# Performance work log

Hardware: AMD Instinct MI355X
Metric: run time of the kernel (lower is better)

Reference implementation:

```python
import jax, jax.numpy as jnp
import numpy as np
import math

DIM = 2048
N_HEADS = 16
N_KV_HEADS = 8
HEAD_DIM = DIM // N_HEADS  # 128
N_REP = N_HEADS // N_KV_HEADS  # 2
BLOCK = 128
TOPK = 8
NEG_INF = -10000.0
SEQ = 4096
BS = 1


def _rope_tables(seq_len, head_dim, base=10000.0):
    inv_freq = 1.0 / (base ** (jnp.arange(0, head_dim, 2, dtype=jnp.float32) / head_dim))
    ang = jnp.arange(seq_len, dtype=jnp.float32)[:, None] * inv_freq[None, :]  # [S, hd/2]
    return jnp.cos(ang), jnp.sin(ang)


def _apply_rope(t, cos, sin):
    # t: [bs, S, h, hd]; interleaved pairs
    t1 = t[..., 0::2]
    t2 = t[..., 1::2]
    c = cos[None, :, None, :]
    s = sin[None, :, None, :]
    out_even = t1 * c - t2 * s
    out_odd = t1 * s + t2 * c
    out = jnp.stack([out_even, out_odd], axis=-1)  # [bs,S,h,hd/2,2]
    return out.reshape(t.shape)


def setup_inputs() -> dict:
    key = jax.random.key(0)
    ks = jax.random.split(key, 5)
    scale = 1.0 / math.sqrt(DIM)
    x = jax.random.normal(ks[0], (BS, SEQ, DIM), dtype=jnp.float32)
    wq = jax.random.normal(ks[1], (DIM, N_HEADS * HEAD_DIM), dtype=jnp.float32) * scale
    wk = jax.random.normal(ks[2], (DIM, N_KV_HEADS * HEAD_DIM), dtype=jnp.float32) * scale
    wv = jax.random.normal(ks[3], (DIM, N_KV_HEADS * HEAD_DIM), dtype=jnp.float32) * scale
    wo = jax.random.normal(ks[4], (DIM, DIM), dtype=jnp.float32) * scale
    return {"x": x, "wq": wq, "wk": wk, "wv": wv, "wo": wo}


def reference(x, wq, wk, wv, wo):
    bs, S, _ = x.shape
    inv_sqrt_d = 1.0 / math.sqrt(HEAD_DIM)

    q = (x @ wq).reshape(bs, S, N_HEADS, HEAD_DIM)
    k = (x @ wk).reshape(bs, S, N_KV_HEADS, HEAD_DIM)
    v = (x @ wv).reshape(bs, S, N_KV_HEADS, HEAD_DIM)

    cos, sin = _rope_tables(S, HEAD_DIM)
    q = _apply_rope(q, cos, sin)
    k = _apply_rope(k, cos, sin)

    # [bs, h, S, hd]
    q = jnp.transpose(q, (0, 2, 1, 3))
    k = jnp.transpose(k, (0, 2, 1, 3))
    v = jnp.transpose(v, (0, 2, 1, 3))

    # GQA expand (repeat_interleave over head dim)
    k_e = jnp.repeat(k, N_REP, axis=1)
    v_e = jnp.repeat(v, N_REP, axis=1)

    num_blocks = S // BLOCK  # 32, divides evenly (pad_len == 0)
    k_blocks = k_e.reshape(bs, N_HEADS, num_blocks, BLOCK, HEAD_DIM)
    block_means = k_blocks.mean(axis=3)  # [bs,h,nb,hd]

    gating = jnp.einsum('bhsd,bhnd->bhsn', q, block_means) * inv_sqrt_d
    q_block_idx = jnp.arange(S) // BLOCK
    future_block = q_block_idx[:, None] < jnp.arange(num_blocks)[None, :]  # [S, nb]
    gating = jnp.where(future_block[None, None], NEG_INF, gating)

    curr_k = min(TOPK, num_blocks)
    _, sel_idx = jax.lax.top_k(gating, curr_k)  # [bs,h,S,k]
    selected = jnp.sum(jax.nn.one_hot(sel_idx, num_blocks, dtype=jnp.float32), axis=-2) > 0  # [bs,h,S,nb]

    token_keep = jnp.repeat(selected, BLOCK, axis=-1)[..., :S]  # [bs,h,S,S]
    token_mask = jnp.where(token_keep, 0.0, NEG_INF)

    scores = jnp.einsum('bhsd,bhtd->bhst', q, k_e) * inv_sqrt_d
    causal = jnp.triu(jnp.ones((S, S), dtype=jnp.float32), k=1)  # 1 where future token
    # faithful to source: elementwise max of token mask and causal*neg_inf
    final_mask = jnp.maximum(token_mask, causal[None, None] * NEG_INF)
    scores = scores + final_mask

    probs = jax.nn.softmax(scores.astype(jnp.float32), axis=-1).astype(scores.dtype)
    out = jnp.einsum('bhst,bhtd->bhsd', probs, v_e)
    out = jnp.transpose(out, (0, 2, 1, 3)).reshape(bs, S, N_HEADS * HEAD_DIM)
    return out @ wo
```

## Files before the change

kernel.cpp:

```cpp
#include <hip/hip_runtime.h>
#include <hip/hip_fp16.h>

#define SQ   4096
#define DIMM 2048
#define QKVN 4096

typedef unsigned short u16;
typedef unsigned int u32;
typedef __attribute__((ext_vector_type(8))) short    short8;
typedef __attribute__((ext_vector_type(8))) _Float16 half8;
typedef __attribute__((ext_vector_type(4))) float    f32x4;

__device__ __forceinline__ u16 f2bf(float f) {
  u32 u = __float_as_uint(f);
  u32 r = u + 0x7fffu + ((u >> 16) & 1u);
  return (u16)(r >> 16);
}
__device__ __forceinline__ float bf2f(u16 h) { return __uint_as_float(((u32)h) << 16); }
__device__ __forceinline__ u16 f2h(float f) { return __half_as_ushort(__float2half(f)); }
__device__ __forceinline__ float h2f(u16 h) { union { u16 u; _Float16 f; } c; c.u = h; return (float)c.f; }

__device__ __forceinline__ void gll16(const void* g, void* l) {
  __builtin_amdgcn_global_load_lds((const __attribute__((address_space(1))) void*)g,
                                   (__attribute__((address_space(3))) void*)l, 16, 0, 0);
}

__device__ __host__ __forceinline__ int cidx(int qb) {
  return qb < 8 ? qb : qb < 16 ? 8 + (qb - 8) * 2 : qb < 24 ? 24 + (qb - 16) * 3 : 48 + (qb - 24) * 4;
}

__global__ __launch_bounds__(256) void k_tables(float* __restrict__ cosb, float* __restrict__ sinb) {
  int idx = blockIdx.x * 256 + threadIdx.x;
  int pos = idx >> 6, i = idx & 63;
  double f = 1.0 / pow(10000.0, (double)i / 64.0);
  float inv = (float)f;
  float ang = (float)pos * inv;
  cosb[idx] = (float)cos((double)ang);
  sinb[idx] = (float)sin((double)ang);
}

__global__ __launch_bounds__(256) void k_split_x(const float* __restrict__ x,
                                                 u16* __restrict__ xh, u16* __restrict__ xl) {
  size_t base = ((size_t)blockIdx.x * 256 + threadIdx.x) * 4;
  float4 v = *(const float4*)(x + base);
  float vv[4] = {v.x, v.y, v.z, v.w};
  u16 hh[4], ll[4];
#pragma unroll
  for (int j = 0; j < 4; j++) {
    hh[j] = f2bf(vv[j]);
    ll[j] = f2bf(vv[j] - bf2f(hh[j]));
  }
  *(uint2*)(xh + base) = make_uint2((u32)hh[0] | ((u32)hh[1] << 16), (u32)hh[2] | ((u32)hh[3] << 16));
  *(uint2*)(xl + base) = make_uint2((u32)ll[0] | ((u32)ll[1] << 16), (u32)ll[2] | ((u32)ll[3] << 16));
}

__global__ __launch_bounds__(256) void k_trans_split(const float* __restrict__ src, int N,
                                                     u16* __restrict__ dh, u16* __restrict__ dl,
                                                     int rowOff) {
  __shared__ float t[64][65];
  int n0 = blockIdx.x * 64, k0 = blockIdx.y * 64;
  int tid = threadIdx.x;
  int c = tid & 63, r4 = tid >> 6;
#pragma unroll
  for (int it = 0; it < 16; it++) {
    int kk = it * 4 + r4;
    t[kk][c] = src[(size_t)(k0 + kk) * N + n0 + c];
  }
  __syncthreads();
#pragma unroll
  for (int it = 0; it < 16; it++) {
    int nn = it * 4 + r4;
    float v = t[c][nn];
    u16 hh = f2bf(v);
    size_t o = (size_t)(rowOff + n0 + nn) * 2048 + k0 + c;
    dh[o] = hh;
    dl[o] = f2bf(v - bf2f(hh));
  }
}

__global__ __launch_bounds__(256) void k_trans_f16(const float* __restrict__ src, int N,
                                                   u16* __restrict__ dst) {
  __shared__ float t[64][65];
  int n0 = blockIdx.x * 64, k0 = blockIdx.y * 64;
  int tid = threadIdx.x;
  int c = tid & 63, r4 = tid >> 6;
#pragma unroll
  for (int it = 0; it < 16; it++) {
    int kk = it * 4 + r4;
    t[kk][c] = src[(size_t)(k0 + kk) * N + n0 + c];
  }
  __syncthreads();
#pragma unroll
  for (int it = 0; it < 16; it++) {
    int nn = it * 4 + r4;
    dst[(size_t)(n0 + nn) * 2048 + k0 + c] = f2h(t[c][nn]);
  }
}

__global__ __launch_bounds__(256) void k_gemm_qkv(
    const u16* __restrict__ xh, const u16* __restrict__ xl,
    const u16* __restrict__ wth, const u16* __restrict__ wtl,
    float* __restrict__ qkv) {
  __shared__ u16 lds[4 * 128 * 64];
  const int tid = threadIdx.x;
  const int lane = tid & 63, wid = tid >> 6;
  const int rg = lane >> 4, c16 = lane & 15;
  const int bid0 = blockIdx.y * 32 + blockIdx.x;
  const int swz = (bid0 & 7) * 128 + (bid0 >> 3);
  const int m0 = (swz >> 5) * 128, n0 = (swz & 31) * 128;
  const int wm = wid >> 1, wn = wid & 1;
  const u16* gsrc = (wid == 0) ? xh + (size_t)m0 * 2048
                  : (wid == 1) ? xl + (size_t)m0 * 2048
                  : (wid == 2) ? wth + (size_t)n0 * 2048
                               : wtl + (size_t)n0 * 2048;
  u16* ldsm = lds + wid * 8192;
  const int sr = lane >> 3, scn = lane & 7;

  f32x4 acc[4][4];
#pragma unroll
  for (int a = 0; a < 4; a++)
#pragma unroll
    for (int b = 0; b < 4; b++) acc[a][b] = (f32x4){0.f, 0.f, 0.f, 0.f};

  for (int k0 = 0; k0 < 2048; k0 += 64) {
#pragma unroll
    for (int i = 0; i < 16; i++) {
      int r = i * 8 + sr;
      int cs = (scn ^ (r & 7)) * 8;
      gll16(gsrc + (size_t)r * 2048 + k0 + cs, ldsm + i * 512);
    }
    __syncthreads();
#pragma unroll
    for (int kk = 0; kk < 2; kk++) {
      short8 ah[4], al[4], bh[4], bl[4];
      int ch = kk * 4 + rg;
#pragma unroll
      for (int mf = 0; mf < 4; mf++) {
        int m = wm * 64 + mf * 16 + c16;
        int off = m * 64 + ((ch ^ (m & 7)) * 8);
        ah[mf] = *(const short8*)(lds + off);
        al[mf] = *(const short8*)(lds + 8192 + off);
      }
#pragma unroll
      for (int nf = 0; nf < 4; nf++) {
        int n = wn * 64 + nf * 16 + c16;
        int off = n * 64 + ((ch ^ (n & 7)) * 8);
        bh[nf] = *(const short8*)(lds + 16384 + off);
        bl[nf] = *(const short8*)(lds + 24576 + off);
      }
#pragma unroll
      for (int mf = 0; mf < 4; mf++)
#pragma unroll
        for (int nf = 0; nf < 4; nf++) {
          acc[mf][nf] = __builtin_amdgcn_mfma_f32_16x16x32_bf16(ah[mf], bh[nf], acc[mf][nf], 0, 0, 0);
          acc[mf][nf] = __builtin_amdgcn_mfma_f32_16x16x32_bf16(ah[mf], bl[nf], acc[mf][nf], 0, 0, 0);
          acc[mf][nf] = __builtin_amdgcn_mfma_f32_16x16x32_bf16(al[mf], bh[nf], acc[mf][nf], 0, 0, 0);
        }
    }
    __syncthreads();
  }
#pragma unroll
  for (int mf = 0; mf < 4; mf++)
#pragma unroll
    for (int nf = 0; nf < 4; nf++)
#pragma unroll
      for (int j = 0; j < 4; j++) {
        int m = m0 + wm * 64 + mf * 16 + rg * 4 + j;
        int n = n0 + wn * 64 + nf * 16 + c16;
        qkv[(size_t)m * QKVN + n] = acc[mf][nf][j];
      }
}

__global__ __launch_bounds__(256) void k_rope_qk(const float* __restrict__ qkv,
                                                 const float* __restrict__ cosb,
                                                 const float* __restrict__ sinb,
                                                 u16* __restrict__ qf, u16* __restrict__ kf2) {
  int idx = blockIdx.x * 256 + threadIdx.x;
  int i = idx & 63;
  int th = idx >> 6;
  int h = th % 24, t = th / 24;
  int c0 = (h < 16) ? h * 128 + 2 * i : 2048 + (h - 16) * 128 + 2 * i;
  float2 eo = *(const float2*)(qkv + (size_t)t * QKVN + c0);
  float c = cosb[t * 64 + i], s = sinb[t * 64 + i];
  float re = eo.x * c - eo.y * s;
  float ro = eo.x * s + eo.y * c;
  if (h < 16) {
    const float QSC = (float)(1.4426950408889634 * 0.08838834764831843);
    u32 pk = (u32)f2h(re * QSC) | ((u32)f2h(ro * QSC) << 16);
    *(u32*)(qf + ((size_t)h * SQ + t) * 128 + 2 * i) = pk;
  } else {
    int hk = h - 16;
    int d = 2 * i;
    int tile = t >> 6, tok = t & 63;
    int kk = tok >> 5, t5 = tok & 31;
    int hf = (t5 >> 2) & 1, c16v = ((t5 >> 3) << 2) | (t5 & 3);
    int dk = d >> 5, rg = (d >> 3) & 3, e = d & 7;
    int lane = rg * 16 + c16v, f = (kk * 2 + hf) * 4 + dk;
    u32 pk = (u32)f2h(re) | ((u32)f2h(ro) << 16);
    *(u32*)(kf2 + ((size_t)((hk * 64 + tile) * 16 + f) * 64 + lane) * 8 + e) = pk;
  }
}

__global__ __launch_bounds__(64) void k_bm(const float* __restrict__ qkv,
                                           const float* __restrict__ cosb,
                                           const float* __restrict__ sinb,
                                           float* __restrict__ bm) {
  int hk = blockIdx.x >> 5, n = blockIdx.x & 31;
  int i = threadIdx.x;
  double se = 0.0, so = 0.0;
  for (int t = 0; t < 128; t++) {
    int tt = n * 128 + t;
    float2 eo = *(const float2*)(qkv + (size_t)tt * QKVN + 2048 + hk * 128 + 2 * i);
    float c = cosb[tt * 64 + i], s = sinb[tt * 64 + i];
    se += (double)(eo.x * c - eo.y * s);
    so += (double)(eo.x * s + eo.y * c);
  }
  float* o = bm + ((size_t)(hk * 32 + n)) * 128 + 2 * i;
  o[0] = (float)(se * (1.0 / 128.0));
  o[1] = (float)(so * (1.0 / 128.0));
}

__global__ __launch_bounds__(64) void k_gate(const float* __restrict__ qkv,
                                             const float* __restrict__ cosb,
                                             const float* __restrict__ sinb,
                                             const float* __restrict__ bm,
                                             unsigned char* __restrict__ sel) {
  __shared__ float q[64][129];
  __shared__ float bml[32 * 128];
  int bz = blockIdx.x;
  int h = bz / 48;
  int rem = bz % 48;
  int b = 8 + (rem >> 1);
  int half = rem & 1;
  int tid = threadIdx.x;
  int hk = h >> 1;
  for (int rr = 0; rr < 64; rr++) {
    int ss = b * 128 + half * 64 + rr;
    float2 eo = *(const float2*)(qkv + (size_t)ss * QKVN + h * 128 + 2 * tid);
    float c = cosb[ss * 64 + tid], sn = sinb[ss * 64 + tid];
    q[rr][2 * tid]     = eo.x * c - eo.y * sn;
    q[rr][2 * tid + 1] = eo.x * sn + eo.y * c;
  }
  for (int o = tid; o < (b + 1) * 128; o += 64) bml[o] = bm[(size_t)hk * 32 * 128 + o];
  __syncthreads();
  int s = b * 128 + half * 64 + tid;
  double gb = 0.0;
  for (int d = 0; d < 128; d++) gb += (double)q[tid][d] * (double)bml[b * 128 + d];
  int cnt = 0;
  for (int n = 0; n < b; n++) {
    double g = 0.0;
    for (int d = 0; d < 128; d++) g += (double)q[tid][d] * (double)bml[n * 128 + d];
    cnt += (g >= gb) ? 1 : 0;
  }
  sel[h * SQ + s] = (cnt <= 7) ? 1 : 0;
}

__global__ __launch_bounds__(256) void k_vt2(const float* __restrict__ qkv, u16* __restrict__ vt2) {
  int hk = blockIdx.x & 7, tile = blockIdx.x >> 3;
  int tid = threadIdx.x;
  u16* dst = vt2 + (size_t)(hk * 64 + tile) * 8192;
#pragma unroll
  for (int rep = 0; rep < 16; rep++) {
    int idx = rep * 256 + tid;
    int tp = idx >> 7;
    int d  = idx & 127;
    int t  = tile * 64 + tp * 2;
    float v0 = qkv[(size_t)t * QKVN + 3072 + hk * 128 + d];
    float v1 = qkv[(size_t)(t + 1) * QKVN + 3072 + hk * 128 + d];
    int tok = tp * 2;
    int kk = tok >> 5, rg = (tok >> 3) & 3, e = tok & 7;
    int nf = d >> 4, c16v = d & 15;
    int lane = rg * 16 + c16v, g = kk * 8 + nf;
    u32 pk = (u32)f2h(v0) | ((u32)f2h(v1) << 16);
    *(u32*)(dst + ((size_t)(g * 64 + lane)) * 8 + e) = pk;
  }
}

__global__ __launch_bounds__(256) void k_attn_chunk(
    const u16* __restrict__ qf, const u16* __restrict__ kf2, const u16* __restrict__ vt2,
    const unsigned char* __restrict__ sel, u16* __restrict__ po, float* __restrict__ ml) {
  __shared__ u16 lds[2][8192];
  const int L = blockIdx.x;
  const int hk = L & 7;
  const int c = L >> 3;
  const int h = hk * 2 + (c & 1);
  const int cc = c >> 1;
  int qb, chunk;
  if (cc < 8)       { qb = cc;                   chunk = 0; }
  else if (cc < 24) { qb = 8 + ((cc - 8) >> 1);  chunk = (cc - 8) & 1; }
  else if (cc < 48) { qb = 16 + (cc - 24) / 3;   chunk = (cc - 24) % 3; }
  else              { qb = 24 + ((cc - 48) >> 2); chunk = (cc - 48) & 3; }
  const int nt128 = (qb < 8) ? 8 : (qb + 1);
  const int t0 = chunk * 32;
  const int t1 = (t0 + 32 < nt128 * 4) ? t0 + 32 : nt128 * 4;
  const int tid = threadIdx.x;
  const int lane = tid & 63, wid = tid >> 6;
  const int rg = lane >> 4, c16 = lane & 15;
  const bool hasMask = (qb >= 8);

  half8 aq[2][4];
#pragma unroll
  for (int mi = 0; mi < 2; mi++)
#pragma unroll
    for (int dk = 0; dk < 4; dk++) {
      int srow = qb * 128 + wid * 32 + mi * 16 + c16;
      aq[mi][dk] = *(const half8*)(qf + ((size_t)h * SQ + srow) * 128 + dk * 32 + rg * 8);
    }

  bool os2[2] = {true, true};
  if (hasMask) {
#pragma unroll
    for (int mi = 0; mi < 2; mi++)
      os2[mi] = sel[h * SQ + qb * 128 + wid * 32 + mi * 16 + c16] != 0;
  }

  f32x4 accO[2][8];
#pragma unroll
  for (int mi = 0; mi < 2; mi++)
#pragma unroll
    for (int nf = 0; nf < 8; nf++) accO[mi][nf] = (f32x4){0.f, 0.f, 0.f, 0.f};
  float mrun[2] = {-1e30f, -1e30f}, lrun[2] = {0.f, 0.f};

  const u16* kbase = kf2 + (size_t)hk * 64 * 8192;
  const u16* vbase = vt2 + (size_t)hk * 64 * 8192;

  auto stage = [&](int b, int n) {
    const u16* ks = kbase + (size_t)n * 4096;
    const u16* vs = vbase + (size_t)n * 4096;
#pragma unroll
    for (int r = 0; r < 2; r++) {
      gll16(ks + r * 2048 + wid * 512 + lane * 8, &lds[b][r * 2048 + wid * 512]);
      gll16(vs + r * 2048 + wid * 512 + lane * 8, &lds[b][4096 + r * 2048 + wid * 512]);
    }
  };

  stage(0, t0);

  for (int n = t0; n < t1; n++) {
    const int cur = (n - t0) & 1;
    __syncthreads();
    if (n + 1 < t1) stage(cur ^ 1, n + 1);
    const u16* lb = &lds[cur][0];

    f32x4 st[2][2];
#pragma unroll
    for (int hf = 0; hf < 2; hf++)
#pragma unroll
      for (int mi = 0; mi < 2; mi++) st[hf][mi] = (f32x4){0.f, 0.f, 0.f, 0.f};

    __builtin_amdgcn_s_setprio(1);
#pragma unroll
    for (int hf = 0; hf < 2; hf++) {
      half8 ka[4];
#pragma unroll
      for (int dk = 0; dk < 4; dk++)
        ka[dk] = *(const half8*)(lb + (hf * 4 + dk) * 512 + lane * 8);
#pragma unroll
      for (int dk = 0; dk < 4; dk++) {
        st[hf][0] = __builtin_amdgcn_mfma_f32_16x16x32_f16(ka[dk], aq[0][dk], st[hf][0], 0, 0, 0);
        st[hf][1] = __builtin_amdgcn_mfma_f32_16x16x32_f16(ka[dk], aq[1][dk], st[hf][1], 0, 0, 0);
      }
    }
    __builtin_amdgcn_s_setprio(0);

    if (hasMask && n >= 4 * qb) {
#pragma unroll
      for (int mi = 0; mi < 2; mi++) {
        if (!os2[mi]) {
          int row = qb * 128 + wid * 32 + mi * 16 + c16;
#pragma unroll
          for (int hf = 0; hf < 2; hf++)
#pragma unroll
            for (int j = 0; j < 4; j++) {
              int tg = n * 32 + rg * 8 + hf * 4 + j;
              if (tg > row) st[hf][mi][j] = -1e30f;
            }
        }
      }
    }

#pragma unroll
    for (int mi = 0; mi < 2; mi++) {
      float mt = st[0][mi][0];
#pragma unroll
      for (int hf = 0; hf < 2; hf++)
#pragma unroll
        for (int j = 0; j < 4; j++)
          if (hf | j) mt = fmaxf(mt, st[hf][mi][j]);
      mt = fmaxf(mt, __shfl_xor(mt, 16, 64));
      mt = fmaxf(mt, __shfl_xor(mt, 32, 64));
      if (!__all(mt <= mrun[mi] + 8.f)) {
        float mnew = fmaxf(mrun[mi], mt);
        float sc = exp2f(mrun[mi] - mnew);
        mrun[mi] = mnew;
        lrun[mi] *= sc;
#pragma unroll
        for (int nf = 0; nf < 8; nf++) accO[mi][nf] *= sc;
      }
      float ps = 0.f;
#pragma unroll
      for (int hf = 0; hf < 2; hf++)
#pragma unroll
        for (int j = 0; j < 4; j++) {
          float p = exp2f(st[hf][mi][j] - mrun[mi]);
          st[hf][mi][j] = p;
          ps += p;
        }
      ps += __shfl_xor(ps, 16, 64);
      ps += __shfl_xor(ps, 32, 64);
      lrun[mi] += ps;
    }

    half8 pa[2];
#pragma unroll
    for (int mi = 0; mi < 2; mi++) {
      union { half8 v; _Float16 e[8]; } pu;
#pragma unroll
      for (int hf = 0; hf < 2; hf++)
#pragma unroll
        for (int j = 0; j < 4; j++)
          pu.e[hf * 4 + j] = (_Float16)st[hf][mi][j];
      pa[mi] = pu.v;
    }

    __builtin_amdgcn_s_setprio(1);
#pragma unroll
    for (int nf = 0; nf < 8; nf++) {
      half8 va = *(const half8*)(lb + 4096 + nf * 512 + lane * 8);
      accO[0][nf] = __builtin_amdgcn_mfma_f32_16x16x32_f16(va, pa[0], accO[0][nf], 0, 0, 0);
      accO[1][nf] = __builtin_amdgcn_mfma_f32_16x16x32_f16(va, pa[1], accO[1][nf], 0, 0, 0);
    }
    __builtin_amdgcn_s_setprio(0);
  }

  const int pidx = h * 80 + cidx(qb) + chunk;
  u16* pob = po + (size_t)pidx * 16384;
#pragma unroll
  for (int mi = 0; mi < 2; mi++) {
    float inv = 1.0f / lrun[mi];
    int row = wid * 32 + mi * 16 + c16;
#pragma unroll
    for (int nf = 0; nf < 8; nf++) {
      u32 p0 = (u32)f2h(accO[mi][nf][0] * inv) | ((u32)f2h(accO[mi][nf][1] * inv) << 16);
      u32 p1 = (u32)f2h(accO[mi][nf][2] * inv) | ((u32)f2h(accO[mi][nf][3] * inv) << 16);
      *(uint2*)&pob[row * 128 + nf * 16 + rg * 4] = make_uint2(p0, p1);
    }
    if (rg == 0)
      ml[(size_t)pidx * 128 + row] = mrun[mi] + log2f(lrun[mi]);
  }
}

__global__ __launch_bounds__(256) void k_attn_combine(
    const u16* __restrict__ po, const float* __restrict__ ml, u16* __restrict__ attn) {
  const int qb = blockIdx.x, h = blockIdx.y;
  const int nc = (qb < 8) ? 1 : (qb < 16) ? 2 : (qb < 24) ? 3 : 4;
  const int base = h * 80 + cidx(qb);
  const int tid = threadIdx.x;
  const int r = tid >> 1, h64 = (tid & 1) * 64;
  float mp[4], M = -1e30f;
#pragma unroll
  for (int ci = 0; ci < 4; ci++) {
    mp[ci] = (ci < nc) ? ml[(size_t)(base + ci) * 128 + r] : -1e30f;
    M = fmaxf(M, mp[ci]);
  }
  float w[4], Ws = 0.f;
#pragma unroll
  for (int ci = 0; ci < 4; ci++) { w[ci] = exp2f(mp[ci] - M); Ws += (ci < nc) ? w[ci] : 0.f; }
  float inv = 1.0f / Ws;
  for (int d = 0; d < 64; d += 4) {
    float a[4] = {0.f, 0.f, 0.f, 0.f};
#pragma unroll
    for (int ci = 0; ci < 4; ci++) {
      if (ci < nc) {
        uint2 u = *(const uint2*)&po[(size_t)(base + ci) * 16384 + r * 128 + h64 + d];
        a[0] += w[ci] * h2f((u16)(u.x & 0xffff));
        a[1] += w[ci] * h2f((u16)(u.x >> 16));
        a[2] += w[ci] * h2f((u16)(u.y & 0xffff));
        a[3] += w[ci] * h2f((u16)(u.y >> 16));
      }
    }
    u32 p0 = (u32)f2h(a[0] * inv) | ((u32)f2h(a[1] * inv) << 16);
    u32 p1 = (u32)f2h(a[2] * inv) | ((u32)f2h(a[3] * inv) << 16);
    *(uint2*)&attn[(size_t)(qb * 128 + r) * DIMM + h * 128 + h64 + d] = make_uint2(p0, p1);
  }
}

__global__ __launch_bounds__(256) void k_gemm_out(
    const u16* __restrict__ attn, const u16* __restrict__ wot, float* __restrict__ out) {
  __shared__ u16 lds[2 * 128 * 64];
  const int tid = threadIdx.x;
  const int lane = tid & 63, wid = tid >> 6;
  const int rg = lane >> 4, c16 = lane & 15;
  const int bid0 = blockIdx.y * 16 + blockIdx.x;
  const int swz = (bid0 & 7) * 64 + (bid0 >> 3);
  const int m0 = (swz >> 4) * 128, n0 = (swz & 15) * 128;
  const int wm = wid >> 1, wn = wid & 1;
  const u16* gsrc = (wid < 2) ? attn + (size_t)m0 * 2048 : wot + (size_t)n0 * 2048;
  const int sr = lane >> 3, scn = lane & 7;

  f32x4 acc[4][4];
#pragma unroll
  for (int a = 0; a < 4; a++)
#pragma unroll
    for (int b = 0; b < 4; b++) acc[a][b] = (f32x4){0.f, 0.f, 0.f, 0.f};

  for (int k0 = 0; k0 < 2048; k0 += 64) {
#pragma unroll
    for (int i = 0; i < 8; i++) {
      int slot = wid * 8 + i;
      int s2 = slot & 15;
      int r = s2 * 8 + sr;
      int cs = (scn ^ (r & 7)) * 8;
      gll16(gsrc + (size_t)r * 2048 + k0 + cs, lds + slot * 512);
    }
    __syncthreads();
#pragma unroll
    for (int kk = 0; kk < 2; kk++) {
      half8 a[4], b[4];
      int ch = kk * 4 + rg;
#pragma unroll
      for (int mf = 0; mf < 4; mf++) {
        int m = wm * 64 + mf * 16 + c16;
        a[mf] = *(const half8*)(lds + m * 64 + ((ch ^ (m & 7)) * 8));
      }
#pragma unroll
      for (int nf = 0; nf < 4; nf++) {
        int n = wn * 64 + nf * 16 + c16;
        b[nf] = *(const half8*)(lds + 8192 + n * 64 + ((ch ^ (n & 7)) * 8));
      }
#pragma unroll
      for (int mf = 0; mf < 4; mf++)
#pragma unroll
        for (int nf = 0; nf < 4; nf++)
          acc[mf][nf] = __builtin_amdgcn_mfma_f32_16x16x32_f16(a[mf], b[nf], acc[mf][nf], 0, 0, 0);
    }
    __syncthreads();
  }
#pragma unroll
  for (int mf = 0; mf < 4; mf++)
#pragma unroll
    for (int nf = 0; nf < 4; nf++)
#pragma unroll
      for (int j = 0; j < 4; j++) {
        int m = m0 + wm * 64 + mf * 16 + rg * 4 + j;
        int n = n0 + wn * 64 + nf * 16 + c16;
        out[(size_t)m * DIMM + n] = acc[mf][nf][j];
      }
}

extern "C" void kernel_launch(void* const* d_in, const int* in_sizes, int n_in,
                              void* d_out, int out_size, void* d_ws, size_t ws_size,
                              hipStream_t stream) {
  (void)in_sizes; (void)n_in; (void)out_size; (void)ws_size;
  const float* x  = (const float*)d_in[0];
  const float* wq = (const float*)d_in[1];
  const float* wk = (const float*)d_in[2];
  const float* wv = (const float*)d_in[3];
  const float* wo = (const float*)d_in[4];
  float* out = (float*)d_out;

  char* ws = (char*)d_ws;
  const size_t MB = 1024 * 1024;
  char* A = ws;
  u16*   xh  = (u16*)(A);
  u16*   xl  = (u16*)(A + 16 * MB);
  u16*   wth = (u16*)(A + 32 * MB);
  u16*   wtl = (u16*)(A + 48 * MB);
  float* qkv = (float*)(A + 64 * MB);
  u16*   po  = (u16*)(A);
  float* ml  = (float*)(A + 48 * MB);
  char* B = ws + 128 * MB;
  size_t off = 0;
  auto alloc = [&](size_t b) { char* p = B + off; off += (b + 255) & ~(size_t)255; return p; };
  u16*   wot  = (u16*)alloc((size_t)DIMM * DIMM * 2);
  float* cosb = (float*)alloc((size_t)SQ * 64 * 4);
  float* sinb = (float*)alloc((size_t)SQ * 64 * 4);
  u16*   qf   = (u16*)alloc((size_t)16 * SQ * 128 * 2);
  u16*   kf2  = (u16*)alloc((size_t)8 * SQ * 128 * 2);
  u16*   vt2  = (u16*)alloc((size_t)8 * 128 * SQ * 2);
  float* bm   = (float*)alloc((size_t)8 * 32 * 128 * 4);
  unsigned char* sel = (unsigned char*)alloc((size_t)16 * SQ);
  u16*   attn = (u16*)alloc((size_t)SQ * DIMM * 2);

  k_tables<<<SQ * 64 / 256, 256, 0, stream>>>(cosb, sinb);
  k_split_x<<<(SQ * DIMM) / (256 * 4), 256, 0, stream>>>(x, xh, xl);
  k_trans_split<<<dim3(32, 32), 256, 0, stream>>>(wq, 2048, wth, wtl, 0);
  k_trans_split<<<dim3(16, 32), 256, 0, stream>>>(wk, 1024, wth, wtl, 2048);
  k_trans_split<<<dim3(16, 32), 256, 0, stream>>>(wv, 1024, wth, wtl, 3072);
  k_trans_f16<<<dim3(32, 32), 256, 0, stream>>>(wo, 2048, wot);
  k_gemm_qkv<<<dim3(32, 32), 256, 0, stream>>>(xh, xl, wth, wtl, qkv);
  k_rope_qk<<<(SQ * 24 * 64) / 256, 256, 0, stream>>>(qkv, cosb, sinb, qf, kf2);
  k_vt2<<<512, 256, 0, stream>>>(qkv, vt2);
  k_bm<<<256, 64, 0, stream>>>(qkv, cosb, sinb, bm);
  k_gate<<<16 * 48, 64, 0, stream>>>(qkv, cosb, sinb, bm, sel);
  k_attn_chunk<<<1280, 256, 0, stream>>>(qf, kf2, vt2, sel, po, ml);
  k_attn_combine<<<dim3(32, 16), 256, 0, stream>>>(po, ml, attn);
  k_gemm_out<<<dim3(16, 32), 256, 0, stream>>>(attn, wot, out);
}
```

Before: 568.6 us.

## Double-buffer QKV GEMM LDS staging and coalesce K/V fragment writes

The QKV GEMM now uses two LDS buffers with a K-step of 32, prefetching the next stage while computing the current one. It drops one barrier per iteration, remaps blocks per XCD for L2 locality and raises wave priority around the MFMA section. The K rope and V layout kernels are rewritten to gather inputs and emit full 16-byte coalesced stores instead of scattered 4-byte writes, with V staged through shared memory. Q rope is split into its own kernel, which adds one launch.

```diff
diff --git a/kernel.cpp b/kernel.cpp
--- a/kernel.cpp
+++ b/kernel.cpp
@@ -101,20 +101,21 @@
     const u16* __restrict__ xh, const u16* __restrict__ xl,
     const u16* __restrict__ wth, const u16* __restrict__ wtl,
     float* __restrict__ qkv) {
-  __shared__ u16 lds[4 * 128 * 64];
+  __shared__ u16 lds[2][16384];
   const int tid = threadIdx.x;
   const int lane = tid & 63, wid = tid >> 6;
   const int rg = lane >> 4, c16 = lane & 15;
   const int bid0 = blockIdx.y * 32 + blockIdx.x;
-  const int swz = (bid0 & 7) * 128 + (bid0 >> 3);
-  const int m0 = (swz >> 5) * 128, n0 = (swz & 31) * 128;
+  const int xcd = bid0 & 7, local = bid0 >> 3;
+  const int m0 = (xcd * 4 + (local & 3)) * 128;
+  const int n0 = (local >> 2) * 128;
   const int wm = wid >> 1, wn = wid & 1;
   const u16* gsrc = (wid == 0) ? xh + (size_t)m0 * 2048
                   : (wid == 1) ? xl + (size_t)m0 * 2048
                   : (wid == 2) ? wth + (size_t)n0 * 2048
                                : wtl + (size_t)n0 * 2048;
-  u16* ldsm = lds + wid * 8192;
-  const int sr = lane >> 3, scn = lane & 7;
+  const int srow4 = lane >> 2;
+  const int pc = lane & 3;
 
   f32x4 acc[4][4];
 #pragma unroll
@@ -122,42 +123,47 @@
 #pragma unroll
     for (int b = 0; b < 4; b++) acc[a][b] = (f32x4){0.f, 0.f, 0.f, 0.f};
 
-  for (int k0 = 0; k0 < 2048; k0 += 64) {
-#pragma unroll
-    for (int i = 0; i < 16; i++) {
-      int r = i * 8 + sr;
-      int cs = (scn ^ (r & 7)) * 8;
-      gll16(gsrc + (size_t)r * 2048 + k0 + cs, ldsm + i * 512);
-    }
+  auto stage = [&](int b, int k0) {
+#pragma unroll
+    for (int i = 0; i < 8; i++) {
+      int r = i * 16 + srow4;
+      int cl = pc ^ ((r >> 1) & 3);
+      gll16(gsrc + (size_t)r * 2048 + k0 + cl * 8, &lds[b][wid * 4096 + i * 512 + lane * 8]);
+    }
+  };
+
+  stage(0, 0);
+
+  for (int ks = 0; ks < 64; ks++) {
     __syncthreads();
-#pragma unroll
-    for (int kk = 0; kk < 2; kk++) {
-      short8 ah[4], al[4], bh[4], bl[4];
-      int ch = kk * 4 + rg;
-#pragma unroll
-      for (int mf = 0; mf < 4; mf++) {
-        int m = wm * 64 + mf * 16 + c16;
-        int off = m * 64 + ((ch ^ (m & 7)) * 8);
-        ah[mf] = *(const short8*)(lds + off);
-        al[mf] = *(const short8*)(lds + 8192 + off);
-      }
+    if (ks + 1 < 64) stage((ks & 1) ^ 1, (ks + 1) * 32);
+    const u16* lb = lds[ks & 1];
+
+    short8 ah[4], al[4], bh[4], bl[4];
+#pragma unroll
+    for (int mf = 0; mf < 4; mf++) {
+      int m = wm * 64 + mf * 16 + c16;
+      int xo = m * 32 + ((rg ^ ((m >> 1) & 3)) * 8);
+      ah[mf] = *(const short8*)(lb + xo);
+      al[mf] = *(const short8*)(lb + 4096 + xo);
+    }
+#pragma unroll
+    for (int nf = 0; nf < 4; nf++) {
+      int n = wn * 64 + nf * 16 + c16;
+      int xo = n * 32 + ((rg ^ ((n >> 1) & 3)) * 8);
+      bh[nf] = *(const short8*)(lb + 8192 + xo);
+      bl[nf] = *(const short8*)(lb + 12288 + xo);
+    }
+    __builtin_amdgcn_s_setprio(1);
+#pragma unroll
+    for (int mf = 0; mf < 4; mf++)
 #pragma unroll
       for (int nf = 0; nf < 4; nf++) {
-        int n = wn * 64 + nf * 16 + c16;
-        int off = n * 64 + ((ch ^ (n & 7)) * 8);
-        bh[nf] = *(const short8*)(lds + 16384 + off);
-        bl[nf] = *(const short8*)(lds + 24576 + off);
-      }
-#pragma unroll
-      for (int mf = 0; mf < 4; mf++)
-#pragma unroll
-        for (int nf = 0; nf < 4; nf++) {
-          acc[mf][nf] = __builtin_amdgcn_mfma_f32_16x16x32_bf16(ah[mf], bh[nf], acc[mf][nf], 0, 0, 0);
-          acc[mf][nf] = __builtin_amdgcn_mfma_f32_16x16x32_bf16(ah[mf], bl[nf], acc[mf][nf], 0, 0, 0);
-          acc[mf][nf] = __builtin_amdgcn_mfma_f32_16x16x32_bf16(al[mf], bh[nf], acc[mf][nf], 0, 0, 0);
-        }
-    }
-    __syncthreads();
+        acc[mf][nf] = __builtin_amdgcn_mfma_f32_16x16x32_bf16(ah[mf], bh[nf], acc[mf][nf], 0, 0, 0);
+        acc[mf][nf] = __builtin_amdgcn_mfma_f32_16x16x32_bf16(ah[mf], bl[nf], acc[mf][nf], 0, 0, 0);
+        acc[mf][nf] = __builtin_amdgcn_mfma_f32_16x16x32_bf16(al[mf], bh[nf], acc[mf][nf], 0, 0, 0);
+      }
+    __builtin_amdgcn_s_setprio(0);
   }
 #pragma unroll
   for (int mf = 0; mf < 4; mf++)
@@ -171,33 +177,54 @@
       }
 }
 
-__global__ __launch_bounds__(256) void k_rope_qk(const float* __restrict__ qkv,
-                                                 const float* __restrict__ cosb,
-                                                 const float* __restrict__ sinb,
-                                                 u16* __restrict__ qf, u16* __restrict__ kf2) {
+__global__ __launch_bounds__(256) void k_rope_q(const float* __restrict__ qkv,
+                                                const float* __restrict__ cosb,
+                                                const float* __restrict__ sinb,
+                                                u16* __restrict__ qf) {
   int idx = blockIdx.x * 256 + threadIdx.x;
   int i = idx & 63;
   int th = idx >> 6;
-  int h = th % 24, t = th / 24;
-  int c0 = (h < 16) ? h * 128 + 2 * i : 2048 + (h - 16) * 128 + 2 * i;
-  float2 eo = *(const float2*)(qkv + (size_t)t * QKVN + c0);
+  int h = th & 15, t = th >> 4;
+  float2 eo = *(const float2*)(qkv + (size_t)t * QKVN + h * 128 + 2 * i);
   float c = cosb[t * 64 + i], s = sinb[t * 64 + i];
-  float re = eo.x * c - eo.y * s;
-  float ro = eo.x * s + eo.y * c;
-  if (h < 16) {
-    const float QSC = (float)(1.4426950408889634 * 0.08838834764831843);
-    u32 pk = (u32)f2h(re * QSC) | ((u32)f2h(ro * QSC) << 16);
-    *(u32*)(qf + ((size_t)h * SQ + t) * 128 + 2 * i) = pk;
-  } else {
-    int hk = h - 16;
-    int d = 2 * i;
-    int tile = t >> 6, tok = t & 63;
-    int kk = tok >> 5, t5 = tok & 31;
-    int hf = (t5 >> 2) & 1, c16v = ((t5 >> 3) << 2) | (t5 & 3);
-    int dk = d >> 5, rg = (d >> 3) & 3, e = d & 7;
-    int lane = rg * 16 + c16v, f = (kk * 2 + hf) * 4 + dk;
-    u32 pk = (u32)f2h(re) | ((u32)f2h(ro) << 16);
-    *(u32*)(kf2 + ((size_t)((hk * 64 + tile) * 16 + f) * 64 + lane) * 8 + e) = pk;
+  const float QSC = (float)(1.4426950408889634 * 0.08838834764831843);
+  float re = (eo.x * c - eo.y * s) * QSC;
+  float ro = (eo.x * s + eo.y * c) * QSC;
+  *(u32*)(qf + ((size_t)h * SQ + t) * 128 + 2 * i) = (u32)f2h(re) | ((u32)f2h(ro) << 16);
+}
+
+__global__ __launch_bounds__(256) void k_rope_kf(const float* __restrict__ qkv,
+                                                 const float* __restrict__ cosb,
+                                                 const float* __restrict__ sinb,
+                                                 u16* __restrict__ kf2) {
+  int hk = blockIdx.x & 7, tile = blockIdx.x >> 3;
+  int tid = threadIdx.x;
+  u16* dst = kf2 + (size_t)(hk * 64 + tile) * 8192;
+#pragma unroll
+  for (int rep = 0; rep < 4; rep++) {
+    int p = rep * 256 + tid;
+    int f = p >> 6, lane = p & 63;
+    int dk = f & 3, hf = (f >> 2) & 1, kk = f >> 3;
+    int rg = lane >> 4, c16v = lane & 15;
+    int t5 = ((c16v >> 2) << 3) | (hf << 2) | (c16v & 3);
+    int t = tile * 64 + kk * 32 + t5;
+    int d0 = dk * 32 + rg * 8;
+    const float* src = qkv + (size_t)t * QKVN + 2048 + hk * 128 + d0;
+    float4 a = *(const float4*)src;
+    float4 b = *(const float4*)(src + 4);
+    int i0 = d0 >> 1;
+    float4 cs = *(const float4*)(cosb + t * 64 + i0);
+    float4 sn = *(const float4*)(sinb + t * 64 + i0);
+    float xe[4] = {a.x, a.z, b.x, b.z}, xo[4] = {a.y, a.w, b.y, b.w};
+    float cc[4] = {cs.x, cs.y, cs.z, cs.w}, ss[4] = {sn.x, sn.y, sn.z, sn.w};
+    u32 pk[4];
+#pragma unroll
+    for (int jj = 0; jj < 4; jj++) {
+      float re = xe[jj] * cc[jj] - xo[jj] * ss[jj];
+      float ro = xe[jj] * ss[jj] + xo[jj] * cc[jj];
+      pk[jj] = (u32)f2h(re) | ((u32)f2h(ro) << 16);
+    }
+    *(uint4*)(dst + (size_t)p * 8) = make_uint4(pk[0], pk[1], pk[2], pk[3]);
   }
 }
 
@@ -256,23 +283,35 @@
 }
 
 __global__ __launch_bounds__(256) void k_vt2(const float* __restrict__ qkv, u16* __restrict__ vt2) {
+  __shared__ float vb[64][129];
   int hk = blockIdx.x & 7, tile = blockIdx.x >> 3;
   int tid = threadIdx.x;
+  int r4 = tid >> 6, cl = (tid & 63) * 2;
+#pragma unroll
+  for (int it = 0; it < 16; it++) {
+    int row = it * 4 + r4;
+    float2 v = *(const float2*)(qkv + (size_t)(tile * 64 + row) * QKVN + 3072 + hk * 128 + cl);
+    vb[row][cl] = v.x;
+    vb[row][cl + 1] = v.y;
+  }
+  __syncthreads();
   u16* dst = vt2 + (size_t)(hk * 64 + tile) * 8192;
 #pragma unroll
-  for (int rep = 0; rep < 16; rep++) {
-    int idx = rep * 256 + tid;
-    int tp = idx >> 7;
-    int d  = idx & 127;
-    int t  = tile * 64 + tp * 2;
-    float v0 = qkv[(size_t)t * QKVN + 3072 + hk * 128 + d];
-    float v1 = qkv[(size_t)(t + 1) * QKVN + 3072 + hk * 128 + d];
-    int tok = tp * 2;
-    int kk = tok >> 5, rg = (tok >> 3) & 3, e = tok & 7;
-    int nf = d >> 4, c16v = d & 15;
-    int lane = rg * 16 + c16v, g = kk * 8 + nf;
-    u32 pk = (u32)f2h(v0) | ((u32)f2h(v1) << 16);
-    *(u32*)(dst + ((size_t)(g * 64 + lane)) * 8 + e) = pk;
+  for (int rep = 0; rep < 4; rep++) {
+    int p = rep * 256 + tid;
+    int g = p >> 6, lane = p & 63;
+    int nf = g & 7, kk = g >> 3;
+    int rg = lane >> 4, c16v = lane & 15;
+    int d = nf * 16 + c16v;
+    int tokb = kk * 32 + rg * 8;
+    u32 pk[4];
+#pragma unroll
+    for (int jj = 0; jj < 4; jj++) {
+      float v0 = vb[tokb + 2 * jj][d];
+      float v1 = vb[tokb + 2 * jj + 1][d];
+      pk[jj] = (u32)f2h(v0) | ((u32)f2h(v1) << 16);
+    }
+    *(uint4*)(dst + (size_t)p * 8) = make_uint4(pk[0], pk[1], pk[2], pk[3]);
   }
 }
 
@@ -589,7 +628,8 @@
   k_trans_split<<<dim3(16, 32), 256, 0, stream>>>(wv, 1024, wth, wtl, 3072);
   k_trans_f16<<<dim3(32, 32), 256, 0, stream>>>(wo, 2048, wot);
   k_gemm_qkv<<<dim3(32, 32), 256, 0, stream>>>(xh, xl, wth, wtl, qkv);
-  k_rope_qk<<<(SQ * 24 * 64) / 256, 256, 0, stream>>>(qkv, cosb, sinb, qf, kf2);
+  k_rope_q<<<(SQ * 16 * 64) / 256, 256, 0, stream>>>(qkv, cosb, sinb, qf);
+  k_rope_kf<<<512, 256, 0, stream>>>(qkv, cosb, sinb, kf2);
   k_vt2<<<512, 256, 0, stream>>>(qkv, vt2);
   k_bm<<<256, 64, 0, stream>>>(qkv, cosb, sinb, bm);
   k_gate<<<16 * 48, 64, 0, stream>>>(qkv, cosb, sinb, bm, sel);
```

New measurement: 582.0 us. 1.02x slower.
